# Optimization experiments

Measured on AMD Instinct MI355X. Metric: run time of the kernel, lower is better.

Reference implementation:

```python
import jax, jax.numpy as jnp
import numpy as np

B, T, D = 16, 2048, 1024


def setup_inputs() -> dict:
    key = jax.random.key(0)
    k1, k2, k3 = jax.random.split(key, 3)
    # scale k and w so the cumulative exp-decay state stays finite in fp32
    k = jax.random.normal(k1, (B, T, D), dtype=jnp.float32) * 0.5
    v = jax.random.normal(k2, (B, T, D), dtype=jnp.float32)
    w = jax.random.normal(k3, (B, T, D), dtype=jnp.float32) * 0.05 - 0.1
    return {"k": k, "v": v, "w": w}


def reference(k, v, w):
    # RWKV-style WKV recurrence, unrolled over the time axis with lax.scan.
    #   a_t = exp(w_t) * a_{t-1} + exp(k_t)
    #   b_t = exp(w_t) * b_{t-1} + exp(k_t) * v_t
    #   out_t = b_t / a_t
    # k, v, w: [B, T, D]; state a, b: [B, D]; initial state zeros (torch buffers).
    ek = jnp.exp(k)
    ew = jnp.exp(w)

    def step(carry, xs):
        a, b = carry
        ew_t, ek_t, v_t = xs  # each [B, D]
        a = ew_t * a + ek_t
        b = ew_t * b + ek_t * v_t
        return (a, b), b / a

    xs = (ew.transpose(1, 0, 2), ek.transpose(1, 0, 2), v.transpose(1, 0, 2))  # [T, B, D]
    bsz, _, dim = k.shape
    init = (jnp.zeros((bsz, dim), dtype=k.dtype), jnp.zeros((bsz, dim), dtype=k.dtype))
    _, out = jax.lax.scan(step, init, xs)  # out: [T, B, D]
    return out.transpose(1, 0, 2)  # [B, T, D]
```

## Files before the change

### kernel.cpp

```cpp
#include <hip/hip_runtime.h>


#define TT 2048
#define DD 1024
#define UU 16

__global__ __launch_bounds__(64) void wkv_fwd(const float* __restrict__ kg,
                                              const float* __restrict__ vg,
                                              const float* __restrict__ wg,
                                              float* __restrict__ og) {
    const int c = blockIdx.x * 64 + threadIdx.x;
    const size_t base = (size_t)(c >> 10) * (size_t)TT * DD
                      + (size_t)(c & (DD - 1));
    const float* kp = kg + base;
    const float* vp = vg + base;
    const float* wp = wg + base;
    float*       op = og + base;

    float kA[UU], vA[UU], wA[UU];
    float kB[UU], vB[UU], wB[UU];

#pragma unroll
    for (int j = 0; j < UU; ++j) {
        const size_t off = (size_t)j * DD;
        kA[j] = kp[off];
        vA[j] = vp[off];
        wA[j] = wp[off];
    }

    float a = 0.0f, b = 0.0f;

    for (int t0 = 0; t0 < TT; t0 += 2 * UU) {
#pragma unroll
        for (int j = 0; j < UU; ++j) {
            const size_t off = (size_t)(t0 + UU + j) * DD;
            kB[j] = kp[off];
            vB[j] = vp[off];
            wB[j] = wp[off];
        }
#pragma unroll
        for (int j = 0; j < UU; ++j) {
            const float ew = __expf(wA[j]);
            const float ek = __expf(kA[j]);
            a = ew * a + ek;
            b = ew * b + ek * vA[j];
            op[(size_t)(t0 + j) * DD] = __fdividef(b, a);
        }
        if (t0 + 2 * UU < TT) {
#pragma unroll
            for (int j = 0; j < UU; ++j) {
                const size_t off = (size_t)(t0 + 2 * UU + j) * DD;
                kA[j] = kp[off];
                vA[j] = vp[off];
                wA[j] = wp[off];
            }
        }
#pragma unroll
        for (int j = 0; j < UU; ++j) {
            const float ew = __expf(wB[j]);
            const float ek = __expf(kB[j]);
            a = ew * a + ek;
            b = ew * b + ek * vB[j];
            op[(size_t)(t0 + UU + j) * DD] = __fdividef(b, a);
        }
    }
}

extern "C" void kernel_launch(void* const* d_in, const int* in_sizes, int n_in,
                              void* d_out, int out_size, void* d_ws, size_t ws_size,
                              hipStream_t stream) {
    const float* k = (const float*)d_in[0];
    const float* v = (const float*)d_in[1];
    const float* w = (const float*)d_in[2];
    float* out = (float*)d_out;

    const int channels = 16 * DD;
    wkv_fwd<<<dim3(channels / 64), dim3(64), 0, stream>>>(k, v, w, out);
}
```

Baseline: 485.8 us.

## Split WKV scan into time chunks with two-pass carry propagation

Replaces the single sequential scan per channel with a chunked scan. The first kernel computes, for each time chunk, the decay product and the partial a/b state; the second kernel combines earlier chunks' summaries to get the starting state, then recomputes outputs within its chunk. This aims to expose 16x more parallel work so the GPU is not limited to one wave per CU on a latency-bound recurrence. The cost is reading k/v/w twice, extra exp work, and a small workspace. The decay product can also change numerical behaviour slightly.

After: 482.9 us. About the same (-0.6%).

```diff
diff --git a/kernel.cpp b/kernel.cpp
--- a/kernel.cpp
+++ b/kernel.cpp
@@ -1,9 +1,143 @@
 #include <hip/hip_runtime.h>
 
 
-#define TT 2048
-#define DD 1024
-#define UU 16
+#define TT   2048
+#define DD   1024
+#define BB   16
+#define BDCH (BB * DD)
+#define NC   16
+#define LL   (TT / NC)
+#define NTH  256
+#define UU   8
+
+__global__ __launch_bounds__(NTH) void wkv_part(const float* __restrict__ kg,
+                                                const float* __restrict__ vg,
+                                                const float* __restrict__ wg,
+                                                float* __restrict__ wsP,
+                                                float* __restrict__ wsA,
+                                                float* __restrict__ wsB) {
+    const int g  = blockIdx.x * NTH + threadIdx.x;
+    const int ch = blockIdx.y;
+    const size_t base = (size_t)(g >> 10) * (size_t)TT * DD
+                      + (size_t)ch * LL * DD
+                      + (size_t)(g & (DD - 1));
+    const float* kp = kg + base;
+    const float* vp = vg + base;
+    const float* wp = wg + base;
+
+    float kA[UU], vA[UU], wA[UU];
+    float kB[UU], vB[UU], wB[UU];
+
+#pragma unroll
+    for (int j = 0; j < UU; ++j) {
+        const size_t off = (size_t)j * DD;
+        kA[j] = kp[off]; vA[j] = vp[off]; wA[j] = wp[off];
+    }
+
+    float P = 1.0f, A = 0.0f, Bv = 0.0f;
+
+    for (int t0 = 0; t0 < LL; t0 += 2 * UU) {
+#pragma unroll
+        for (int j = 0; j < UU; ++j) {
+            const size_t off = (size_t)(t0 + UU + j) * DD;
+            kB[j] = kp[off]; vB[j] = vp[off]; wB[j] = wp[off];
+        }
+#pragma unroll
+        for (int j = 0; j < UU; ++j) {
+            const float ew = __expf(wA[j]);
+            const float ek = __expf(kA[j]);
+            P  = P * ew;
+            A  = ew * A  + ek;
+            Bv = ew * Bv + ek * vA[j];
+        }
+        if (t0 + 2 * UU < LL) {
+#pragma unroll
+            for (int j = 0; j < UU; ++j) {
+                const size_t off = (size_t)(t0 + 2 * UU + j) * DD;
+                kA[j] = kp[off]; vA[j] = vp[off]; wA[j] = wp[off];
+            }
+        }
+#pragma unroll
+        for (int j = 0; j < UU; ++j) {
+            const float ew = __expf(wB[j]);
+            const float ek = __expf(kB[j]);
+            P  = P * ew;
+            A  = ew * A  + ek;
+            Bv = ew * Bv + ek * vB[j];
+        }
+    }
+
+    const int idx = ch * BDCH + g;
+    wsP[idx] = P;
+    wsA[idx] = A;
+    wsB[idx] = Bv;
+}
+
+__global__ __launch_bounds__(NTH) void wkv_final(const float* __restrict__ kg,
+                                                 const float* __restrict__ vg,
+                                                 const float* __restrict__ wg,
+                                                 float* __restrict__ og,
+                                                 const float* __restrict__ wsP,
+                                                 const float* __restrict__ wsA,
+                                                 const float* __restrict__ wsB) {
+    const int g  = blockIdx.x * NTH + threadIdx.x;
+    const int ch = blockIdx.y;
+    const size_t base = (size_t)(g >> 10) * (size_t)TT * DD
+                      + (size_t)ch * LL * DD
+                      + (size_t)(g & (DD - 1));
+    const float* kp = kg + base;
+    const float* vp = vg + base;
+    const float* wp = wg + base;
+    float*       op = og + base;
+
+    float a = 0.0f, b = 0.0f;
+    for (int cc = 0; cc < ch; ++cc) {
+        const int idx = cc * BDCH + g;
+        const float P = wsP[idx];
+        a = P * a + wsA[idx];
+        b = P * b + wsB[idx];
+    }
+
+    float kA[UU], vA[UU], wA[UU];
+    float kB[UU], vB[UU], wB[UU];
+
+#pragma unroll
+    for (int j = 0; j < UU; ++j) {
+        const size_t off = (size_t)j * DD;
+        kA[j] = kp[off]; vA[j] = vp[off]; wA[j] = wp[off];
+    }
+
+    for (int t0 = 0; t0 < LL; t0 += 2 * UU) {
+#pragma unroll
+        for (int j = 0; j < UU; ++j) {
+            const size_t off = (size_t)(t0 + UU + j) * DD;
+            kB[j] = kp[off]; vB[j] = vp[off]; wB[j] = wp[off];
+        }
+#pragma unroll
+        for (int j = 0; j < UU; ++j) {
+            const float ew = __expf(wA[j]);
+            const float ek = __expf(kA[j]);
+            a = ew * a + ek;
+            b = ew * b + ek * vA[j];
+            op[(size_t)(t0 + j) * DD] = __fdividef(b, a);
+        }
+        if (t0 + 2 * UU < LL) {
+#pragma unroll
+            for (int j = 0; j < UU; ++j) {
+                const size_t off = (size_t)(t0 + 2 * UU + j) * DD;
+                kA[j] = kp[off]; vA[j] = vp[off]; wA[j] = wp[off];
+            }
+        }
+#pragma unroll
+        for (int j = 0; j < UU; ++j) {
+            const float ew = __expf(wB[j]);
+            const float ek = __expf(kB[j]);
+            a = ew * a + ek;
+            b = ew * b + ek * vB[j];
+            op[(size_t)(t0 + UU + j) * DD] = __fdividef(b, a);
+        }
+    }
+}
 
 __global__ __launch_bounds__(64) void wkv_fwd(const float* __restrict__ kg,
                                               const float* __restrict__ vg,
@@ -17,51 +151,45 @@
     const float* wp = wg + base;
     float*       op = og + base;
 
-    float kA[UU], vA[UU], wA[UU];
-    float kB[UU], vB[UU], wB[UU];
-
-#pragma unroll
-    for (int j = 0; j < UU; ++j) {
+    float kA[16], vA[16], wA[16];
+    float kB[16], vB[16], wB[16];
+
+#pragma unroll
+    for (int j = 0; j < 16; ++j) {
         const size_t off = (size_t)j * DD;
-        kA[j] = kp[off];
-        vA[j] = vp[off];
-        wA[j] = wp[off];
+        kA[j] = kp[off]; vA[j] = vp[off]; wA[j] = wp[off];
     }
 
     float a = 0.0f, b = 0.0f;
 
-    for (int t0 = 0; t0 < TT; t0 += 2 * UU) {
-#pragma unroll
-        for (int j = 0; j < UU; ++j) {
-            const size_t off = (size_t)(t0 + UU + j) * DD;
-            kB[j] = kp[off];
-            vB[j] = vp[off];
-            wB[j] = wp[off];
-        }
-#pragma unroll
-        for (int j = 0; j < UU; ++j) {
+    for (int t0 = 0; t0 < TT; t0 += 32) {
+#pragma unroll
+        for (int j = 0; j < 16; ++j) {
+            const size_t off = (size_t)(t0 + 16 + j) * DD;
+            kB[j] = kp[off]; vB[j] = vp[off]; wB[j] = wp[off];
+        }
+#pragma unroll
+        for (int j = 0; j < 16; ++j) {
             const float ew = __expf(wA[j]);
             const float ek = __expf(kA[j]);
             a = ew * a + ek;
             b = ew * b + ek * vA[j];
             op[(size_t)(t0 + j) * DD] = __fdividef(b, a);
         }
-        if (t0 + 2 * UU < TT) {
-#pragma unroll
-            for (int j = 0; j < UU; ++j) {
-                const size_t off = (size_t)(t0 + 2 * UU + j) * DD;
-                kA[j] = kp[off];
-                vA[j] = vp[off];
-                wA[j] = wp[off];
+        if (t0 + 32 < TT) {
+#pragma unroll
+            for (int j = 0; j < 16; ++j) {
+                const size_t off = (size_t)(t0 + 32 + j) * DD;
+                kA[j] = kp[off]; vA[j] = vp[off]; wA[j] = wp[off];
             }
         }
 #pragma unroll
-        for (int j = 0; j < UU; ++j) {
+        for (int j = 0; j < 16; ++j) {
             const float ew = __expf(wB[j]);
             const float ek = __expf(kB[j]);
             a = ew * a + ek;
             b = ew * b + ek * vB[j];
-            op[(size_t)(t0 + UU + j) * DD] = __fdividef(b, a);
+            op[(size_t)(t0 + 16 + j) * DD] = __fdividef(b, a);
         }
     }
 }
@@ -74,6 +202,15 @@
     const float* w = (const float*)d_in[2];
     float* out = (float*)d_out;
 
-    const int channels = 16 * DD;
-    wkv_fwd<<<dim3(channels / 64), dim3(64), 0, stream>>>(k, v, w, out);
-}
+    const size_t need = (size_t)3 * NC * BDCH * sizeof(float);
+    if (d_ws != nullptr && ws_size >= need) {
+        float* wsP = (float*)d_ws;
+        float* wsA = wsP + (size_t)NC * BDCH;
+        float* wsB = wsA + (size_t)NC * BDCH;
+        dim3 grid(BDCH / NTH, NC);
+        wkv_part<<<grid, dim3(NTH), 0, stream>>>(k, v, w, wsP, wsA, wsB);
+        wkv_final<<<grid, dim3(NTH), 0, stream>>>(k, v, w, out, wsP, wsA, wsB);
+    } else {
+        wkv_fwd<<<dim3(BDCH / 64), dim3(64), 0, stream>>>(k, v, w, out);
+    }
+}
```

## Split WKV recurrence into chunked two-pass parallel scan with float4 loads

Applied to the files above, without the earlier changes.

Splits the time axis into 32 chunks. A first kernel computes each chunk's decay product and partial a/b state. A second kernel folds the preceding chunk summaries into a carry-in and rescans its chunk to write outputs, using float4 vectorized accesses. This removes the latency bound of a long sequential scan over few threads, at the cost of reading the inputs twice and needing workspace.

Result: faster. 476.2 us (-2.0%).

```diff
diff --git a/kernel.cpp b/kernel.cpp
--- a/kernel.cpp
+++ b/kernel.cpp
@@ -3,66 +3,190 @@
 
 #define TT 2048
 #define DD 1024
-#define UU 16
+#define BB 16
+#define NC 32
+#define LL (TT / NC)
+#define NTH 256
+#define NG (BB * (DD / 4))
+#define UU 4
+
+__device__ __forceinline__ float4 f4_fold(float4 P, float4 s, float4 add) {
+    return make_float4(fmaf(P.x, s.x, add.x), fmaf(P.y, s.y, add.y),
+                       fmaf(P.z, s.z, add.z), fmaf(P.w, s.w, add.w));
+}
+
+#define K1_STEP_C(c, kk, vv, ww)                                           \
+    do {                                                                   \
+        const float ew = __expf(ww.c);                                     \
+        const float ek = __expf(kk.c);                                     \
+        P.c *= ew;                                                         \
+        A.c = fmaf(ew, A.c, ek);                                           \
+        Bv.c = fmaf(ew, Bv.c, ek * vv.c);                                  \
+    } while (0)
+#define K1_STEP(kk, vv, ww)                                                \
+    {                                                                      \
+        K1_STEP_C(x, kk, vv, ww);                                          \
+        K1_STEP_C(y, kk, vv, ww);                                          \
+        K1_STEP_C(z, kk, vv, ww);                                          \
+        K1_STEP_C(w, kk, vv, ww);                                          \
+    }
+
+#define K3_STEP_C(c, kk, vv, ww, oo)                                       \
+    do {                                                                   \
+        const float ew = __expf(ww.c);                                     \
+        const float ek = __expf(kk.c);                                     \
+        a.c = fmaf(ew, a.c, ek);                                           \
+        bv.c = fmaf(ew, bv.c, ek * vv.c);                                  \
+        oo.c = __fdividef(bv.c, a.c);                                      \
+    } while (0)
+#define K3_STEP(kk, vv, ww, oo)                                            \
+    {                                                                      \
+        K3_STEP_C(x, kk, vv, ww, oo);                                      \
+        K3_STEP_C(y, kk, vv, ww, oo);                                      \
+        K3_STEP_C(z, kk, vv, ww, oo);                                      \
+        K3_STEP_C(w, kk, vv, ww, oo);                                      \
+    }
+
+__global__ __launch_bounds__(NTH) void wkv_part(const float* __restrict__ kg,
+                                                const float* __restrict__ vg,
+                                                const float* __restrict__ wg,
+                                                float4* __restrict__ wsP,
+                                                float4* __restrict__ wsA,
+                                                float4* __restrict__ wsB) {
+    const int b = blockIdx.x;
+    const int ch = blockIdx.y;
+    const size_t base = ((size_t)b * TT + (size_t)ch * LL) * DD + threadIdx.x * 4;
+    const float4* kp = (const float4*)(kg + base);
+    const float4* vp = (const float4*)(vg + base);
+    const float4* wp = (const float4*)(wg + base);
+    const int S = DD / 4;
+
+    float4 kA[UU], vA[UU], wA[UU], kB[UU], vB[UU], wB[UU];
+
+#pragma unroll
+    for (int j = 0; j < UU; ++j) {
+        kA[j] = kp[(size_t)j * S];
+        vA[j] = vp[(size_t)j * S];
+        wA[j] = wp[(size_t)j * S];
+    }
+
+    float4 P = make_float4(1.f, 1.f, 1.f, 1.f);
+    float4 A = make_float4(0.f, 0.f, 0.f, 0.f);
+    float4 Bv = make_float4(0.f, 0.f, 0.f, 0.f);
+
+    for (int t0 = 0; t0 < LL; t0 += 2 * UU) {
+#pragma unroll
+        for (int j = 0; j < UU; ++j) {
+            const size_t off = (size_t)(t0 + UU + j) * S;
+            kB[j] = kp[off]; vB[j] = vp[off]; wB[j] = wp[off];
+        }
+#pragma unroll
+        for (int j = 0; j < UU; ++j) { K1_STEP(kA[j], vA[j], wA[j]); }
+        if (t0 + 2 * UU < LL) {
+#pragma unroll
+            for (int j = 0; j < UU; ++j) {
+                const size_t off = (size_t)(t0 + 2 * UU + j) * S;
+                kA[j] = kp[off]; vA[j] = vp[off]; wA[j] = wp[off];
+            }
+        }
+#pragma unroll
+        for (int j = 0; j < UU; ++j) { K1_STEP(kB[j], vB[j], wB[j]); }
+    }
+
+    const int g = b * (DD / 4) + threadIdx.x;
+    wsP[ch * NG + g] = P;
+    wsA[ch * NG + g] = A;
+    wsB[ch * NG + g] = Bv;
+}
+
+__global__ __launch_bounds__(NTH) void wkv_final(const float* __restrict__ kg,
+                                                 const float* __restrict__ vg,
+                                                 const float* __restrict__ wg,
+                                                 float* __restrict__ og,
+                                                 const float4* __restrict__ wsP,
+                                                 const float4* __restrict__ wsA,
+                                                 const float4* __restrict__ wsB) {
+    const int b = blockIdx.x;
+    const int ch = blockIdx.y;
+    const size_t base = ((size_t)b * TT + (size_t)ch * LL) * DD + threadIdx.x * 4;
+    const float4* kp = (const float4*)(kg + base);
+    const float4* vp = (const float4*)(vg + base);
+    const float4* wp = (const float4*)(wg + base);
+    float4* op = (float4*)(og + base);
+    const int S = DD / 4;
+    const int g = b * (DD / 4) + threadIdx.x;
+
+    float4 a = make_float4(0.f, 0.f, 0.f, 0.f);
+    float4 bv = make_float4(0.f, 0.f, 0.f, 0.f);
+    if (ch > 0) {
+        float4 Pc = wsP[g], Ac = wsA[g], Bc = wsB[g];
+        for (int cc = 1; cc < ch; ++cc) {
+            const float4 Pn = wsP[cc * NG + g];
+            const float4 An = wsA[cc * NG + g];
+            const float4 Bn = wsB[cc * NG + g];
+            a = f4_fold(Pc, a, Ac);
+            bv = f4_fold(Pc, bv, Bc);
+            Pc = Pn; Ac = An; Bc = Bn;
+        }
+        a = f4_fold(Pc, a, Ac);
+        bv = f4_fold(Pc, bv, Bc);
+    }
+
+    float4 kA[UU], vA[UU], wA[UU], kB[UU], vB[UU], wB[UU];
+
+#pragma unroll
+    for (int j = 0; j < UU; ++j) {
+        kA[j] = kp[(size_t)j * S];
+        vA[j] = vp[(size_t)j * S];
+        wA[j] = wp[(size_t)j * S];
+    }
+
+    for (int t0 = 0; t0 < LL; t0 += 2 * UU) {
+#pragma unroll
+        for (int j = 0; j < UU; ++j) {
+            const size_t off = (size_t)(t0 + UU + j) * S;
+            kB[j] = kp[off]; vB[j] = vp[off]; wB[j] = wp[off];
+        }
+#pragma unroll
+        for (int j = 0; j < UU; ++j) {
+            float4 o;
+            K3_STEP(kA[j], vA[j], wA[j], o);
+            op[(size_t)(t0 + j) * S] = o;
+        }
+        if (t0 + 2 * UU < LL) {
+#pragma unroll
+            for (int j = 0; j < UU; ++j) {
+                const size_t off = (size_t)(t0 + 2 * UU + j) * S;
+                kA[j] = kp[off]; vA[j] = vp[off]; wA[j] = wp[off];
+            }
+        }
+#pragma unroll
+        for (int j = 0; j < UU; ++j) {
+            float4 o;
+            K3_STEP(kB[j], vB[j], wB[j], o);
+            op[(size_t)(t0 + UU + j) * S] = o;
+        }
+    }
+}
 
 __global__ __launch_bounds__(64) void wkv_fwd(const float* __restrict__ kg,
                                               const float* __restrict__ vg,
                                               const float* __restrict__ wg,
                                               float* __restrict__ og) {
     const int c = blockIdx.x * 64 + threadIdx.x;
-    const size_t base = (size_t)(c >> 10) * (size_t)TT * DD
-                      + (size_t)(c & (DD - 1));
+    const size_t base = (size_t)(c >> 10) * (size_t)TT * DD + (size_t)(c & (DD - 1));
     const float* kp = kg + base;
     const float* vp = vg + base;
     const float* wp = wg + base;
-    float*       op = og + base;
-
-    float kA[UU], vA[UU], wA[UU];
-    float kB[UU], vB[UU], wB[UU];
-
-#pragma unroll
-    for (int j = 0; j < UU; ++j) {
-        const size_t off = (size_t)j * DD;
-        kA[j] = kp[off];
-        vA[j] = vp[off];
-        wA[j] = wp[off];
-    }
+    float* op = og + base;
 
     float a = 0.0f, b = 0.0f;
-
-    for (int t0 = 0; t0 < TT; t0 += 2 * UU) {
-#pragma unroll
-        for (int j = 0; j < UU; ++j) {
-            const size_t off = (size_t)(t0 + UU + j) * DD;
-            kB[j] = kp[off];
-            vB[j] = vp[off];
-            wB[j] = wp[off];
-        }
-#pragma unroll
-        for (int j = 0; j < UU; ++j) {
-            const float ew = __expf(wA[j]);
-            const float ek = __expf(kA[j]);
-            a = ew * a + ek;
-            b = ew * b + ek * vA[j];
-            op[(size_t)(t0 + j) * DD] = __fdividef(b, a);
-        }
-        if (t0 + 2 * UU < TT) {
-#pragma unroll
-            for (int j = 0; j < UU; ++j) {
-                const size_t off = (size_t)(t0 + 2 * UU + j) * DD;
-                kA[j] = kp[off];
-                vA[j] = vp[off];
-                wA[j] = wp[off];
-            }
-        }
-#pragma unroll
-        for (int j = 0; j < UU; ++j) {
-            const float ew = __expf(wB[j]);
-            const float ek = __expf(kB[j]);
-            a = ew * a + ek;
-            b = ew * b + ek * vB[j];
-            op[(size_t)(t0 + UU + j) * DD] = __fdividef(b, a);
-        }
+    for (int t = 0; t < TT; ++t) {
+        const float ew = __expf(wp[(size_t)t * DD]);
+        const float ek = __expf(kp[(size_t)t * DD]);
+        a = ew * a + ek;
+        b = ew * b + ek * vp[(size_t)t * DD];
+        op[(size_t)t * DD] = __fdividef(b, a);
     }
 }
 
@@ -74,6 +198,14 @@
     const float* w = (const float*)d_in[2];
     float* out = (float*)d_out;
 
-    const int channels = 16 * DD;
-    wkv_fwd<<<dim3(channels / 64), dim3(64), 0, stream>>>(k, v, w, out);
-}
+    const size_t need = (size_t)3 * NC * NG * sizeof(float4);
+    if (d_ws != nullptr && ws_size >= need) {
+        float4* wsP = (float4*)d_ws;
+        float4* wsA = wsP + (size_t)NC * NG;
+        float4* wsB = wsA + (size_t)NC * NG;
+        wkv_part<<<dim3(BB, NC - 1), dim3(NTH), 0, stream>>>(k, v, w, wsP, wsA, wsB);
+        wkv_final<<<dim3(BB, NC), dim3(NTH), 0, stream>>>(k, v, w, out, wsP, wsA, wsB);
+    } else {
+        wkv_fwd<<<dim3((BB * DD) / 64), dim3(64), 0, stream>>>(k, v, w, out);
+    }
+}
```
